# Kernel tuning notes

Measured on AMD Instinct MI355X. Metric: run time of the kernel, lower is better.

## Reference

```python
import jax, jax.numpy as jnp
import numpy as np

N_STEPS = 20      # max(n_steps_al, n_steps_kc)
ALPHA   = 0.9     # membrane decay exp(-dt/tau_m)
V_TH    = 1.0     # spiking threshold
G_SOMA  = 0.3     # dendrite->axon coupling conductance (2-compartment KC)
APL_GAIN = 1.0    # graded APL gain
I_SCALE = 0.5     # graded ORN drive scale
BETA    = 10.0    # surrogate-gradient sharpness ('soft' sigmoid)

@jax.custom_vjp
def spike(x):
    return (x > 0).astype(x.dtype)

def _spike_fwd(x):
    return spike(x), x

def _spike_bwd(x, g):
    s = jax.nn.sigmoid(BETA * x)
    return (g * BETA * s * (1.0 - s),)

spike.defvjp(_spike_fwd, _spike_bwd)


def _sparse_w(key, shape, density):
    k1, k2 = jax.random.split(key)
    mask = jax.random.bernoulli(k1, density, shape)
    w = jax.random.uniform(k2, shape)
    return (mask * w).astype(jnp.float32)


def setup_inputs() -> dict:
    key = jax.random.key(0)
    ks = jax.random.split(key, 10)
    batch, n_or, n_orn, n_ln, n_pn, n_kc, n_odors = 4096, 21, 42, 56, 42, 2000, 34
    or_input = jax.random.uniform(ks[0], (batch, n_or), dtype=jnp.float32)
    or_gains = jnp.ones((n_or,), jnp.float32)
    # fixed OR->ORN mapping: OR i drives left (2i) and right (2i+1) ORNs
    m = np.zeros((n_or, n_orn), np.float32)
    for i in range(n_or):
        m[i, 2 * i] = 1.0
        m[i, 2 * i + 1] = 1.0
    mapping = jnp.asarray(m)
    orn_to_pn = _sparse_w(ks[1], (n_orn, n_pn), 0.3)
    orn_to_ln = _sparse_w(ks[2], (n_orn, n_ln), 0.3)
    ln_to_pn = _sparse_w(ks[3], (n_ln, n_pn), 0.3)
    pn_to_kc = _sparse_w(ks[4], (n_pn, n_kc), 0.15)  # ~6 PN claws per KC
    kc_to_apl = jax.random.uniform(ks[5], (n_kc, 1), dtype=jnp.float32) * 0.01
    apl_to_kc = jax.random.uniform(ks[6], (1, n_kc), dtype=jnp.float32)
    dec_w = jax.random.normal(ks[7], (n_kc, n_odors), dtype=jnp.float32) * 0.02
    dec_b = jnp.zeros((n_odors,), jnp.float32)
    return {"or_input": or_input, "or_gains": or_gains, "mapping": mapping,
            "orn_to_pn": orn_to_pn, "orn_to_ln": orn_to_ln, "ln_to_pn": ln_to_pn,
            "pn_to_kc": pn_to_kc, "kc_to_apl": kc_to_apl, "apl_to_kc": apl_to_kc,
            "dec_w": dec_w, "dec_b": dec_b}


def reference(or_input, or_gains, mapping, orn_to_pn, orn_to_ln, ln_to_pn,
              pn_to_kc, kc_to_apl, apl_to_kc, dec_w, dec_b):
    B = or_input.shape[0]
    n_orn, n_pn = orn_to_pn.shape
    n_ln = orn_to_ln.shape[1]
    n_kc = pn_to_kc.shape[1]
    # OR transduction: graded, learnable per-OR gain
    orn_drive = (or_input * jax.nn.softplus(or_gains)) @ mapping  # [B, n_orn]

    z = lambda n: jnp.zeros((B, n), or_input.dtype)
    carry0 = (z(n_orn), z(n_ln), z(n_pn), z(n_kc), z(n_kc), z(1), z(n_kc))

    def step(carry, _):
        v_orn, v_ln, v_pn, v_d, v_a, apl, kc_cnt = carry
        # ORN LIF driven by graded OR current
        v_orn = ALPHA * v_orn + I_SCALE * orn_drive
        s_orn = spike(v_orn - V_TH)
        v_orn = v_orn * (1.0 - s_orn)
        # LN LIF (lateral inhibition interneurons)
        v_ln = ALPHA * v_ln + s_orn @ orn_to_ln
        s_ln = spike(v_ln - V_TH)
        v_ln = v_ln * (1.0 - s_ln)
        # PN LIF: ORN excitation, LN inhibition
        v_pn = ALPHA * v_pn + s_orn @ orn_to_pn - s_ln @ ln_to_pn
        s_pn = spike(v_pn - V_TH)
        v_pn = v_pn * (1.0 - s_pn)
        # KC 2-compartment: dendrite gets PN input and APL inhibition
        v_d = ALPHA * v_d + s_pn @ pn_to_kc - apl @ apl_to_kc
        v_a = ALPHA * v_a + G_SOMA * (v_d - v_a)
        s_kc = spike(v_a - V_TH)
        v_a = v_a * (1.0 - s_kc)
        # APL: graded (non-spiking) global inhibition from KC spikes
        apl = APL_GAIN * jax.nn.relu(s_kc @ kc_to_apl)
        return (v_orn, v_ln, v_pn, v_d, v_a, apl, kc_cnt + s_kc), None

    carry, _ = jax.lax.scan(step, carry0, None, length=N_STEPS)
    kc_count = carry[-1]
    kc_rates = kc_count / N_STEPS
    logits = kc_rates @ dec_w + dec_b  # [B, n_odors]
    return logits
```

## Files before the change

kernel.cpp:

```cpp
#include <hip/hip_runtime.h>

#define NSTEPS 20
#define ALPHA  0.9f
#define VTH    1.0f
#define GSOMA  0.3f
#define ISCALE 0.5f

#define NOR  21
#define NORN 42
#define NLN  56
#define NPN  42
#define NKC  2000
#define NOD  34

#define TPB  256
#define KPER 8

__global__ __launch_bounds__(TPB)
void snn_all(const float* __restrict__ or_input,
             const float* __restrict__ or_gains,
             const float* __restrict__ mapping,
             const float* __restrict__ orn_to_pn,
             const float* __restrict__ orn_to_ln,
             const float* __restrict__ ln_to_pn,
             const float* __restrict__ pn_to_kc,
             const float* __restrict__ kc_to_apl,
             const float* __restrict__ apl_to_kc,
             const float* __restrict__ dec_w,
             const float* __restrict__ dec_b,
             float* __restrict__ out)
{
    __shared__ ulonglong2 sAB[NSTEPS];
    __shared__ unsigned long long sPN[NSTEPS];
    __shared__ float sRed[2][4];
    __shared__ float sRed2[4 * NOD];

    const int tid  = threadIdx.x;
    const int lane = tid & 63;
    const int wid  = tid >> 6;
    const int b    = blockIdx.x;

    if (wid == 0) {
        const int jl = lane < NLN ? lane : 0;
        float wOl[NORN];
#pragma unroll
        for (int o = 0; o < NORN; ++o) wOl[o] = orn_to_ln[o * NLN + jl];

        float spg = 0.f;
        if (lane < NOR) spg = log1pf(expf(or_gains[lane]));

        float drive = 0.f;
        {
            const float* x = or_input + (long)b * NOR;
            const int jo = lane < NORN ? lane : 0;
#pragma unroll
            for (int i = 0; i < NOR; ++i) {
                float g = __shfl(spg, i);
                drive += x[i] * g * mapping[i * NORN + jo];
            }
            drive *= ISCALE;
        }

        float v_orn = 0.f, v_ln = 0.f;
        for (int t = 0; t < NSTEPS; ++t) {
            bool so = false;
            if (lane < NORN) {
                v_orn = ALPHA * v_orn + drive;
                so = (v_orn - VTH) > 0.f;
                if (so) v_orn = 0.f;
            }
            const unsigned long long mOrn = __ballot(so);
            const unsigned int mo_lo = (unsigned int)mOrn;
            const unsigned int mo_hi = (unsigned int)(mOrn >> 32);

            float aln = 0.f;
#pragma unroll
            for (int o = 0; o < 32; ++o) aln += (float)((mo_lo >> o) & 1u) * wOl[o];
#pragma unroll
            for (int o = 32; o < NORN; ++o) aln += (float)((mo_hi >> (o - 32)) & 1u) * wOl[o];

            bool sl = false;
            if (lane < NLN) {
                v_ln = ALPHA * v_ln + aln;
                sl = (v_ln - VTH) > 0.f;
                if (sl) v_ln = 0.f;
            }
            const unsigned long long mLn = __ballot(sl);
            if (lane == 0) sAB[t] = make_ulonglong2(mOrn, mLn);
        }
        asm volatile("" ::: "memory");

        const int jp = lane < NPN ? lane : 0;
        float wOp[NORN];
#pragma unroll
        for (int o = 0; o < NORN; ++o) wOp[o] = orn_to_pn[o * NPN + jp];

        float apn[NSTEPS];
#pragma unroll
        for (int t = 0; t < NSTEPS; ++t) {
            const unsigned long long mo = sAB[t].x;
            const unsigned int lo = (unsigned int)mo;
            const unsigned int hi = (unsigned int)(mo >> 32);
            float a = 0.f;
#pragma unroll
            for (int o = 0; o < 32; ++o) a += (float)((lo >> o) & 1u) * wOp[o];
#pragma unroll
            for (int o = 32; o < NORN; ++o) a += (float)((hi >> (o - 32)) & 1u) * wOp[o];
            apn[t] = a;
        }
        asm volatile("" ::: "memory");

        float wLp[NLN];
#pragma unroll
        for (int l = 0; l < NLN; ++l) wLp[l] = ln_to_pn[l * NPN + jp];

        float v_pn = 0.f;
#pragma unroll
        for (int t = 0; t < NSTEPS; ++t) {
            const unsigned long long ml = sAB[t].y;
            const unsigned int lo = (unsigned int)ml;
            const unsigned int hi = (unsigned int)(ml >> 32);
            float h = 0.f;
#pragma unroll
            for (int l = 0; l < 32; ++l) h += (float)((lo >> l) & 1u) * wLp[l];
#pragma unroll
            for (int l = 32; l < NLN; ++l) h += (float)((hi >> (l - 32)) & 1u) * wLp[l];

            bool sp = false;
            if (lane < NPN) {
                v_pn = ALPHA * v_pn + apn[t] - h;
                sp = (v_pn - VTH) > 0.f;
                if (sp) v_pn = 0.f;
            }
            const unsigned long long mPn = __ballot(sp);
            if (lane == 0) sPN[t] = mPn;
        }
    }

    const int  kbase = tid * KPER;
    const bool act   = (tid < 250);
    float vd[KPER], va[KPER], cnt[KPER], wa2k[KPER], wk2a[KPER];
#pragma unroll
    for (int j = 0; j < KPER; ++j) { vd[j] = 0.f; va[j] = 0.f; cnt[j] = 0.f; }
    {
        const float4* a4 = (const float4*)(apl_to_kc + (act ? kbase : 0));
        const float4* k4 = (const float4*)(kc_to_apl + (act ? kbase : 0));
        float4 a0 = a4[0], a1 = a4[1], k0 = k4[0], k1 = k4[1];
        const float g = act ? 1.f : 0.f;
        wa2k[0] = g * a0.x; wa2k[1] = g * a0.y; wa2k[2] = g * a0.z; wa2k[3] = g * a0.w;
        wa2k[4] = g * a1.x; wa2k[5] = g * a1.y; wa2k[6] = g * a1.z; wa2k[7] = g * a1.w;
        wk2a[0] = g * k0.x; wk2a[1] = g * k0.y; wk2a[2] = g * k0.z; wk2a[3] = g * k0.w;
        wk2a[4] = g * k1.x; wk2a[5] = g * k1.y; wk2a[6] = g * k1.z; wk2a[7] = g * k1.w;
    }
    if (tid < 8) sRed[tid >> 2][tid & 3] = 0.f;
    __syncthreads();

    for (int t = 0; t < NSTEPS; ++t) {
        const float* rp = sRed[(t + 1) & 1];
        const float apl = fmaxf(rp[0] + rp[1] + rp[2] + rp[3], 0.f);

#pragma unroll
        for (int j = 0; j < KPER; ++j) vd[j] = ALPHA * vd[j] - apl * wa2k[j];

        unsigned long long m = sPN[t];
        while (m) {
            const int p0 = __builtin_ctzll(m); m &= m - 1;
            int p1 = p0; float f1 = 0.f;
            if (m) { p1 = __builtin_ctzll(m); m &= m - 1; f1 = 1.f; }
            if (act) {
                const float4* w0 = (const float4*)(pn_to_kc + (long)p0 * NKC + kbase);
                const float4* w1 = (const float4*)(pn_to_kc + (long)p1 * NKC + kbase);
                float4 a0 = w0[0], a1 = w0[1];
                float4 b0 = w1[0], b1 = w1[1];
                vd[0] += a0.x; vd[1] += a0.y; vd[2] += a0.z; vd[3] += a0.w;
                vd[4] += a1.x; vd[5] += a1.y; vd[6] += a1.z; vd[7] += a1.w;
                vd[0] += f1 * b0.x; vd[1] += f1 * b0.y; vd[2] += f1 * b0.z; vd[3] += f1 * b0.w;
                vd[4] += f1 * b1.x; vd[5] += f1 * b1.y; vd[6] += f1 * b1.z; vd[7] += f1 * b1.w;
            }
        }

        float aplp = 0.f;
#pragma unroll
        for (int j = 0; j < KPER; ++j) {
            va[j] = ALPHA * va[j] + GSOMA * (vd[j] - va[j]);
            float s = (va[j] - VTH) > 0.f ? 1.f : 0.f;
            va[j] *= (1.f - s);
            cnt[j] += s;
            aplp += s * wk2a[j];
        }
        for (int off = 32; off > 0; off >>= 1) aplp += __shfl_xor(aplp, off, 64);
        if (lane == 0) sRed[t & 1][wid] = aplp;
        __syncthreads();
    }

    float acc[NOD];
#pragma unroll
    for (int o = 0; o < NOD; ++o) acc[o] = 0.f;
    if (act) {
#pragma unroll
        for (int j = 0; j < KPER; ++j) {
            float r = cnt[j] / 20.0f;
            if (r != 0.f) {
                const float* wr = dec_w + (long)(kbase + j) * NOD;
#pragma unroll
                for (int o = 0; o < NOD; ++o) acc[o] += r * wr[o];
            }
        }
    }
#pragma unroll
    for (int o = 0; o < NOD; ++o) {
        float v = acc[o];
        for (int off = 32; off > 0; off >>= 1) v += __shfl_xor(v, off, 64);
        if (lane == 0) sRed2[wid * NOD + o] = v;
    }
    __syncthreads();
    if (tid < NOD) {
        float v = sRed2[tid] + sRed2[NOD + tid] + sRed2[2 * NOD + tid] +
                  sRed2[3 * NOD + tid] + dec_b[tid];
        out[(long)b * NOD + tid] = v;
    }
}

extern "C" void kernel_launch(void* const* d_in, const int* in_sizes, int n_in,
                              void* d_out, int out_size, void* d_ws, size_t ws_size,
                              hipStream_t stream) {
    (void)n_in; (void)out_size; (void)d_ws; (void)ws_size;
    const float* or_input  = (const float*)d_in[0];
    const float* or_gains  = (const float*)d_in[1];
    const float* mapping   = (const float*)d_in[2];
    const float* orn_to_pn = (const float*)d_in[3];
    const float* orn_to_ln = (const float*)d_in[4];
    const float* ln_to_pn  = (const float*)d_in[5];
    const float* pn_to_kc  = (const float*)d_in[6];
    const float* kc_to_apl = (const float*)d_in[7];
    const float* apl_to_kc = (const float*)d_in[8];
    const float* dec_w     = (const float*)d_in[9];
    const float* dec_b     = (const float*)d_in[10];
    float* out = (float*)d_out;

    const int batch = in_sizes[0] / NOR;
    hipLaunchKernelGGL(snn_all, dim3(batch), dim3(TPB), 0, stream,
                       or_input, or_gains, mapping, orn_to_pn, orn_to_ln,
                       ln_to_pn, pn_to_kc, kc_to_apl, apl_to_kc, dec_w, dec_b, out);
}
```

Baseline: 253.9 us.

## Process two batch rows per block, sharing pn_to_kc loads across rows

Each block now handles two batch rows. The first two wavefronts run the ORN/LN/PN front end in parallel, one per row. The KC stage iterates over the union of both rows' PN spike masks, so each pn_to_kc row loaded is applied to both rows' dendrite states. This halves the block count and the per-step barrier and APL-reduction overhead per row, and it also uses an otherwise idle wavefront for the front end. The cost is doubled register state for the KC neurons, masked multiply-adds where only one row spiked, and a duplicated epilogue with extra syncs.

```diff
diff --git a/kernel.cpp b/kernel.cpp
--- a/kernel.cpp
+++ b/kernel.cpp
@@ -15,32 +15,37 @@
 
 #define TPB  256
 #define KPER 8
+#define RPB  2
 
 __global__ __launch_bounds__(TPB)
-void snn_all(const float* __restrict__ or_input,
-             const float* __restrict__ or_gains,
-             const float* __restrict__ mapping,
-             const float* __restrict__ orn_to_pn,
-             const float* __restrict__ orn_to_ln,
-             const float* __restrict__ ln_to_pn,
-             const float* __restrict__ pn_to_kc,
-             const float* __restrict__ kc_to_apl,
-             const float* __restrict__ apl_to_kc,
-             const float* __restrict__ dec_w,
-             const float* __restrict__ dec_b,
-             float* __restrict__ out)
+void snn_all2(const float* __restrict__ or_input,
+              const float* __restrict__ or_gains,
+              const float* __restrict__ mapping,
+              const float* __restrict__ orn_to_pn,
+              const float* __restrict__ orn_to_ln,
+              const float* __restrict__ ln_to_pn,
+              const float* __restrict__ pn_to_kc,
+              const float* __restrict__ kc_to_apl,
+              const float* __restrict__ apl_to_kc,
+              const float* __restrict__ dec_w,
+              const float* __restrict__ dec_b,
+              float* __restrict__ out,
+              int batch)
 {
-    __shared__ ulonglong2 sAB[NSTEPS];
-    __shared__ unsigned long long sPN[NSTEPS];
-    __shared__ float sRed[2][4];
+    __shared__ ulonglong2 sAB[RPB][NSTEPS];
+    __shared__ unsigned long long sPN[RPB][NSTEPS];
+    __shared__ float sRed[RPB][2][4];
     __shared__ float sRed2[4 * NOD];
 
     const int tid  = threadIdx.x;
     const int lane = tid & 63;
     const int wid  = tid >> 6;
     const int b    = blockIdx.x;
-
-    if (wid == 0) {
+    const int row0 = b * RPB;
+
+    if (wid < RPB && (row0 + wid) < batch) {
+        const int row = row0 + wid;
+
         const int jl = lane < NLN ? lane : 0;
         float wOl[NORN];
 #pragma unroll
@@ -51,7 +56,7 @@
 
         float drive = 0.f;
         {
-            const float* x = or_input + (long)b * NOR;
+            const float* x = or_input + (long)row * NOR;
             const int jo = lane < NORN ? lane : 0;
 #pragma unroll
             for (int i = 0; i < NOR; ++i) {
@@ -86,7 +91,7 @@
                 if (sl) v_ln = 0.f;
             }
             const unsigned long long mLn = __ballot(sl);
-            if (lane == 0) sAB[t] = make_ulonglong2(mOrn, mLn);
+            if (lane == 0) sAB[wid][t] = make_ulonglong2(mOrn, mLn);
         }
         asm volatile("" ::: "memory");
 
@@ -98,7 +103,7 @@
         float apn[NSTEPS];
 #pragma unroll
         for (int t = 0; t < NSTEPS; ++t) {
-            const unsigned long long mo = sAB[t].x;
+            const unsigned long long mo = sAB[wid][t].x;
             const unsigned int lo = (unsigned int)mo;
             const unsigned int hi = (unsigned int)(mo >> 32);
             float a = 0.f;
@@ -117,7 +122,7 @@
         float v_pn = 0.f;
 #pragma unroll
         for (int t = 0; t < NSTEPS; ++t) {
-            const unsigned long long ml = sAB[t].y;
+            const unsigned long long ml = sAB[wid][t].y;
             const unsigned int lo = (unsigned int)ml;
             const unsigned int hi = (unsigned int)(ml >> 32);
             float h = 0.f;
@@ -133,15 +138,22 @@
                 if (sp) v_pn = 0.f;
             }
             const unsigned long long mPn = __ballot(sp);
-            if (lane == 0) sPN[t] = mPn;
-        }
+            if (lane == 0) sPN[wid][t] = mPn;
+        }
+    } else if (wid < RPB) {
+        if (lane < NSTEPS) sPN[wid][lane] = 0ULL;
     }
 
     const int  kbase = tid * KPER;
     const bool act   = (tid < 250);
-    float vd[KPER], va[KPER], cnt[KPER], wa2k[KPER], wk2a[KPER];
-#pragma unroll
-    for (int j = 0; j < KPER; ++j) { vd[j] = 0.f; va[j] = 0.f; cnt[j] = 0.f; }
+    float vd0[KPER], va0[KPER], cnt0[KPER];
+    float vd1[KPER], va1[KPER], cnt1[KPER];
+    float wa2k[KPER], wk2a[KPER];
+#pragma unroll
+    for (int j = 0; j < KPER; ++j) {
+        vd0[j] = 0.f; va0[j] = 0.f; cnt0[j] = 0.f;
+        vd1[j] = 0.f; va1[j] = 0.f; cnt1[j] = 0.f;
+    }
     {
         const float4* a4 = (const float4*)(apl_to_kc + (act ? kbase : 0));
         const float4* k4 = (const float4*)(kc_to_apl + (act ? kbase : 0));
@@ -152,73 +164,107 @@
         wk2a[0] = g * k0.x; wk2a[1] = g * k0.y; wk2a[2] = g * k0.z; wk2a[3] = g * k0.w;
         wk2a[4] = g * k1.x; wk2a[5] = g * k1.y; wk2a[6] = g * k1.z; wk2a[7] = g * k1.w;
     }
-    if (tid < 8) sRed[tid >> 2][tid & 3] = 0.f;
+    if (tid < RPB * 2 * 4) ((float*)sRed)[tid] = 0.f;
     __syncthreads();
 
     for (int t = 0; t < NSTEPS; ++t) {
-        const float* rp = sRed[(t + 1) & 1];
-        const float apl = fmaxf(rp[0] + rp[1] + rp[2] + rp[3], 0.f);
-
-#pragma unroll
-        for (int j = 0; j < KPER; ++j) vd[j] = ALPHA * vd[j] - apl * wa2k[j];
-
-        unsigned long long m = sPN[t];
-        while (m) {
-            const int p0 = __builtin_ctzll(m); m &= m - 1;
-            int p1 = p0; float f1 = 0.f;
-            if (m) { p1 = __builtin_ctzll(m); m &= m - 1; f1 = 1.f; }
+        const float* rp0 = sRed[0][(t + 1) & 1];
+        const float* rp1 = sRed[1][(t + 1) & 1];
+        const float apl0 = fmaxf(rp0[0] + rp0[1] + rp0[2] + rp0[3], 0.f);
+        const float apl1 = fmaxf(rp1[0] + rp1[1] + rp1[2] + rp1[3], 0.f);
+
+#pragma unroll
+        for (int j = 0; j < KPER; ++j) {
+            vd0[j] = ALPHA * vd0[j] - apl0 * wa2k[j];
+            vd1[j] = ALPHA * vd1[j] - apl1 * wa2k[j];
+        }
+
+        const unsigned long long m0 = sPN[0][t];
+        const unsigned long long m1 = sPN[1][t];
+        unsigned long long mu = m0 | m1;
+        while (mu) {
+            const int p0 = __builtin_ctzll(mu); mu &= mu - 1;
+            int p1 = p0; float g1 = 0.f;
+            if (mu) { p1 = __builtin_ctzll(mu); mu &= mu - 1; g1 = 1.f; }
             if (act) {
+                const float f00 = (float)((m0 >> p0) & 1ULL);
+                const float f01 = g1 * (float)((m0 >> p1) & 1ULL);
+                const float f10 = (float)((m1 >> p0) & 1ULL);
+                const float f11 = g1 * (float)((m1 >> p1) & 1ULL);
                 const float4* w0 = (const float4*)(pn_to_kc + (long)p0 * NKC + kbase);
                 const float4* w1 = (const float4*)(pn_to_kc + (long)p1 * NKC + kbase);
                 float4 a0 = w0[0], a1 = w0[1];
                 float4 b0 = w1[0], b1 = w1[1];
-                vd[0] += a0.x; vd[1] += a0.y; vd[2] += a0.z; vd[3] += a0.w;
-                vd[4] += a1.x; vd[5] += a1.y; vd[6] += a1.z; vd[7] += a1.w;
-                vd[0] += f1 * b0.x; vd[1] += f1 * b0.y; vd[2] += f1 * b0.z; vd[3] += f1 * b0.w;
-                vd[4] += f1 * b1.x; vd[5] += f1 * b1.y; vd[6] += f1 * b1.z; vd[7] += f1 * b1.w;
-            }
-        }
-
-        float aplp = 0.f;
+                vd0[0] += f00 * a0.x; vd0[1] += f00 * a0.y; vd0[2] += f00 * a0.z; vd0[3] += f00 * a0.w;
+                vd0[4] += f00 * a1.x; vd0[5] += f00 * a1.y; vd0[6] += f00 * a1.z; vd0[7] += f00 * a1.w;
+                vd0[0] += f01 * b0.x; vd0[1] += f01 * b0.y; vd0[2] += f01 * b0.z; vd0[3] += f01 * b0.w;
+                vd0[4] += f01 * b1.x; vd0[5] += f01 * b1.y; vd0[6] += f01 * b1.z; vd0[7] += f01 * b1.w;
+                vd1[0] += f10 * a0.x; vd1[1] += f10 * a0.y; vd1[2] += f10 * a0.z; vd1[3] += f10 * a0.w;
+                vd1[4] += f10 * a1.x; vd1[5] += f10 * a1.y; vd1[6] += f10 * a1.z; vd1[7] += f10 * a1.w;
+                vd1[0] += f11 * b0.x; vd1[1] += f11 * b0.y; vd1[2] += f11 * b0.z; vd1[3] += f11 * b0.w;
+                vd1[4] += f11 * b1.x; vd1[5] += f11 * b1.y; vd1[6] += f11 * b1.z; vd1[7] += f11 * b1.w;
+            }
+        }
+
+        float aplp0 = 0.f, aplp1 = 0.f;
 #pragma unroll
         for (int j = 0; j < KPER; ++j) {
-            va[j] = ALPHA * va[j] + GSOMA * (vd[j] - va[j]);
-            float s = (va[j] - VTH) > 0.f ? 1.f : 0.f;
-            va[j] *= (1.f - s);
-            cnt[j] += s;
-            aplp += s * wk2a[j];
-        }
-        for (int off = 32; off > 0; off >>= 1) aplp += __shfl_xor(aplp, off, 64);
-        if (lane == 0) sRed[t & 1][wid] = aplp;
+            va0[j] = ALPHA * va0[j] + GSOMA * (vd0[j] - va0[j]);
+            float s0 = (va0[j] - VTH) > 0.f ? 1.f : 0.f;
+            va0[j] *= (1.f - s0);
+            cnt0[j] += s0;
+            aplp0 += s0 * wk2a[j];
+            va1[j] = ALPHA * va1[j] + GSOMA * (vd1[j] - va1[j]);
+            float s1 = (va1[j] - VTH) > 0.f ? 1.f : 0.f;
+            va1[j] *= (1.f - s1);
+            cnt1[j] += s1;
+            aplp1 += s1 * wk2a[j];
+        }
+        for (int off = 32; off > 0; off >>= 1) {
+            aplp0 += __shfl_xor(aplp0, off, 64);
+            aplp1 += __shfl_xor(aplp1, off, 64);
+        }
+        if (lane == 0) {
+            sRed[0][t & 1][wid] = aplp0;
+            sRed[1][t & 1][wid] = aplp1;
+        }
         __syncthreads();
     }
 
-    float acc[NOD];
-#pragma unroll
-    for (int o = 0; o < NOD; ++o) acc[o] = 0.f;
-    if (act) {
-#pragma unroll
-        for (int j = 0; j < KPER; ++j) {
-            float r = cnt[j] / 20.0f;
-            if (r != 0.f) {
-                const float* wr = dec_w + (long)(kbase + j) * NOD;
-#pragma unroll
-                for (int o = 0; o < NOD; ++o) acc[o] += r * wr[o];
-            }
-        }
-    }
-#pragma unroll
-    for (int o = 0; o < NOD; ++o) {
-        float v = acc[o];
-        for (int off = 32; off > 0; off >>= 1) v += __shfl_xor(v, off, 64);
-        if (lane == 0) sRed2[wid * NOD + o] = v;
-    }
-    __syncthreads();
-    if (tid < NOD) {
-        float v = sRed2[tid] + sRed2[NOD + tid] + sRed2[2 * NOD + tid] +
-                  sRed2[3 * NOD + tid] + dec_b[tid];
-        out[(long)b * NOD + tid] = v;
-    }
+#define EPILOG(CNT, ROW)                                                        \
+    do {                                                                        \
+        float acc[NOD];                                                         \
+        _Pragma("unroll")                                                       \
+        for (int o = 0; o < NOD; ++o) acc[o] = 0.f;                             \
+        if (act) {                                                              \
+            _Pragma("unroll")                                                   \
+            for (int j = 0; j < KPER; ++j) {                                    \
+                float r = CNT[j] / 20.0f;                                       \
+                if (r != 0.f) {                                                 \
+                    const float* wr = dec_w + (long)(kbase + j) * NOD;          \
+                    _Pragma("unroll")                                           \
+                    for (int o = 0; o < NOD; ++o) acc[o] += r * wr[o];          \
+                }                                                               \
+            }                                                                   \
+        }                                                                       \
+        _Pragma("unroll")                                                       \
+        for (int o = 0; o < NOD; ++o) {                                         \
+            float v = acc[o];                                                   \
+            for (int off = 32; off > 0; off >>= 1) v += __shfl_xor(v, off, 64); \
+            if (lane == 0) sRed2[wid * NOD + o] = v;                            \
+        }                                                                       \
+        __syncthreads();                                                        \
+        if (tid < NOD && (ROW) < batch) {                                       \
+            float v = sRed2[tid] + sRed2[NOD + tid] + sRed2[2 * NOD + tid] +    \
+                      sRed2[3 * NOD + tid] + dec_b[tid];                        \
+            out[(long)(ROW) * NOD + tid] = v;                                   \
+        }                                                                       \
+        __syncthreads();                                                        \
+    } while (0)
+
+    EPILOG(cnt0, row0);
+    EPILOG(cnt1, row0 + 1);
+#undef EPILOG
 }
 
 extern "C" void kernel_launch(void* const* d_in, const int* in_sizes, int n_in,
@@ -239,7 +285,7 @@
     float* out = (float*)d_out;
 
     const int batch = in_sizes[0] / NOR;
-    hipLaunchKernelGGL(snn_all, dim3(batch), dim3(TPB), 0, stream,
+    hipLaunchKernelGGL(snn_all2, dim3((batch + RPB - 1) / RPB), dim3(TPB), 0, stream,
                        or_input, or_gains, mapping, orn_to_pn, orn_to_ln,
-                       ln_to_pn, pn_to_kc, kc_to_apl, apl_to_kc, dec_w, dec_b, out);
+                       ln_to_pn, pn_to_kc, kc_to_apl, apl_to_kc, dec_w, dec_b, out, batch);
 }
```

Measured after the change: 252.2 us. Within noise of the previous version (-0.7%).
